# Kernel tuning notes

Hardware: AMD Instinct MI355X
Metric: run time of the kernel (lower is better)

The kernel has to match this reference:

```python
import jax, jax.numpy as jnp
import numpy as np

N, F, U, R, B, M = 8192, 64, 64, 4, 20, 512


def setup_inputs() -> dict:
    key = jax.random.key(0)
    ks = jax.random.split(key, 6)
    features = jax.random.normal(ks[0], (1, N, F), dtype=jnp.float32)
    out_indices = jax.random.randint(ks[1], (1, M), 0, N, dtype=jnp.int64)
    # normalized adjacency per relation; scale keeps activations O(1)
    adjacency = jax.random.uniform(ks[2], (R, N, N), dtype=jnp.float32) / N
    bases = jax.random.normal(ks[3], (F, U, B), dtype=jnp.float32) * (1.0 / np.sqrt(F * B))
    coefficients = jax.random.normal(ks[4], (R, B), dtype=jnp.float32)
    self_kernel = jax.random.normal(ks[5], (F, U), dtype=jnp.float32) * (1.0 / np.sqrt(F))
    bias = jnp.zeros((U,), dtype=jnp.float32)
    return {
        "features": features,
        "out_indices": out_indices,
        "adjacency": adjacency,
        "bases": bases,
        "coefficients": coefficients,
        "self_kernel": self_kernel,
        "bias": bias,
    }


def reference(features, out_indices, adjacency, bases, coefficients, self_kernel, bias):
    # features: (1, N, F); adjacency: (R, N, N)
    x = features[0]  # (N, F) -- full-batch, batch dim is 1
    # basis decomposition: W_r = sum_k bases[:, :, k] * coeff[r, k]
    W = jnp.einsum("fuk,rk->rfu", bases, coefficients)  # (R, F, U)
    xw = jnp.einsum("nf,rfu->rnu", x, W)               # (R, N, U)
    agg = jnp.einsum("rnm,rmu->nu", adjacency, xw)      # sum_r A_r @ (X W_r)
    out = agg + x @ self_kernel + bias                   # (N, U)
    out = jax.nn.relu(out)
    # final_layer=False: return all node features with batch dim restored
    return out[None]  # (1, N, U)
```

## Files before the change

### kernel.cpp

```cpp
#include <hip/hip_runtime.h>


typedef float v4f __attribute__((ext_vector_type(4)));
typedef unsigned int v4u __attribute__((ext_vector_type(4)));
typedef short v8s __attribute__((ext_vector_type(8)));

__device__ __forceinline__ unsigned short f2bf(float f) {
  unsigned int u = __builtin_bit_cast(unsigned int, f);
  return (unsigned short)((u + 0x7fffu + ((u >> 16) & 1u)) >> 16);
}

__device__ __forceinline__ void gload16(const void* g, void* l) {
  __builtin_amdgcn_global_load_lds((const __attribute__((address_space(1))) void*)g,
                                   (__attribute__((address_space(3))) void*)l, 16, 0, 0);
}

__global__ __launch_bounds__(256) void rgcn_wk(const float* __restrict__ bases,
                                               const float* __restrict__ coef,
                                               float* __restrict__ W) {
  int i = blockIdx.x * 256 + threadIdx.x;
  int r = i >> 12;
  int fu = i & 4095;
  float s = 0.f;
#pragma unroll
  for (int k = 0; k < 20; ++k) s += bases[fu * 20 + k] * coef[r * 20 + k];
  W[i] = s;
}

__global__ __launch_bounds__(256) void rgcn_prep(const float* __restrict__ x,
                                                 const float* __restrict__ W,
                                                 const float* __restrict__ sk,
                                                 const float* __restrict__ bias,
                                                 unsigned short* __restrict__ xwf,
                                                 float* __restrict__ selfout) {
  __shared__ float lx[2048];
  __shared__ unsigned short lxw[8192];
  const int t = threadIdx.x;
  const int blk = blockIdx.x;
  const int n0 = blk * 32;
  for (int i = t; i < 2048; i += 256) lx[i] = x[(size_t)n0 * 64 + i];
  __syncthreads();
  const int u = t & 63, rq = t >> 6;
  float acc[8][5];
#pragma unroll
  for (int p = 0; p < 8; ++p)
#pragma unroll
    for (int c = 0; c < 5; ++c) acc[p][c] = 0.f;
  const float* wu = W + u;
  const float* sku = sk + u;
#pragma unroll 4
  for (int f = 0; f < 64; ++f) {
    float w0 = wu[f * 64];
    float w1 = wu[4096 + f * 64];
    float w2 = wu[8192 + f * 64];
    float w3 = wu[12288 + f * 64];
    float w4 = sku[f * 64];
#pragma unroll
    for (int p = 0; p < 8; ++p) {
      float xv = lx[(rq * 8 + p) * 64 + f];
      acc[p][0] += xv * w0;
      acc[p][1] += xv * w1;
      acc[p][2] += xv * w2;
      acc[p][3] += xv * w3;
      acc[p][4] += xv * w4;
    }
  }
  const float bu = bias[u];
#pragma unroll
  for (int p = 0; p < 8; ++p) {
    int km = rq * 8 + p;
    selfout[(size_t)(n0 + km) * 64 + u] = acc[p][4] + bu;
    int idx = (u >> 4) * 512 + ((km >> 3) * 16 + (u & 15)) * 8 + (km & 7);
#pragma unroll
    for (int r = 0; r < 4; ++r) lxw[r * 2048 + idx] = f2bf(acc[p][r]);
  }
  __syncthreads();
  const unsigned int* lsrc = (const unsigned int*)lxw;
  unsigned int* gdst = (unsigned int*)xwf;
  for (int i = t; i < 4096; i += 256) {
    int r = i >> 10, q = i & 1023;
    gdst[(size_t)(r * 256 + blk) * 1024 + q] = lsrc[i];
  }
}


#define PACK8(S, X0, X1)          \
  {                               \
    S[0] = (short)f2bf(X0.x);     \
    S[1] = (short)f2bf(X0.y);     \
    S[2] = (short)f2bf(X0.z);     \
    S[3] = (short)f2bf(X0.w);     \
    S[4] = (short)f2bf(X1.x);     \
    S[5] = (short)f2bf(X1.y);     \
    S[6] = (short)f2bf(X1.z);     \
    S[7] = (short)f2bf(X1.w);     \
  }

#define STAGE(P)                                          \
  {                                                       \
    char* stb = smem + (w * 2 + (P)) * 8192;              \
    gload16(aps0, stb);                                   \
    gload16(aps1, stb + 1024);                            \
    gload16(aps2, stb + 2048);                            \
    gload16(aps3, stb + 3072);                            \
    gload16(bpp, stb + 4096);                             \
    gload16(bpp + 512, stb + 5120);                       \
    gload16(bpp + 1024, stb + 6144);                      \
    gload16(bpp + 1536, stb + 7168);                      \
    aps0 += 32; aps1 += 32; aps2 += 32; aps3 += 32;       \
    bpp += 2048;                                          \
  }

#define STEP(P, VMN, DO_STAGE)                                             \
  {                                                                        \
    asm volatile("s_waitcnt vmcnt(" #VMN ")" ::: "memory");                \
    __builtin_amdgcn_sched_barrier(0);                                     \
    const char* sb = smem + (w * 2 + (P)) * 8192;                          \
    v4f a00 = *(const v4f*)(sb + ao00);                                    \
    v4f a01 = *(const v4f*)(sb + ao01);                                    \
    v4f a10 = *(const v4f*)(sb + ao10);                                    \
    v4f a11 = *(const v4f*)(sb + ao11);                                    \
    v4u b0 = *(const v4u*)(sb + bo);                                       \
    v4u b1 = *(const v4u*)(sb + bo + 1024);                                \
    v4u b2 = *(const v4u*)(sb + bo + 2048);                                \
    v4u b3 = *(const v4u*)(sb + bo + 3072);                                \
    asm volatile("s_waitcnt lgkmcnt(0)" ::: "memory");                     \
    __builtin_amdgcn_sched_barrier(0);                                     \
    if (DO_STAGE) STAGE(P)                                                 \
    v8s af0, af1;                                                          \
    PACK8(af0, a00, a01);                                                  \
    PACK8(af1, a10, a11);                                                  \
    v8s bf0 = __builtin_bit_cast(v8s, b0);                                 \
    v8s bf1 = __builtin_bit_cast(v8s, b1);                                 \
    v8s bf2 = __builtin_bit_cast(v8s, b2);                                 \
    v8s bf3 = __builtin_bit_cast(v8s, b3);                                 \
    acc00 = __builtin_amdgcn_mfma_f32_16x16x32_bf16(af0, bf0, acc00, 0, 0, 0); \
    acc01 = __builtin_amdgcn_mfma_f32_16x16x32_bf16(af0, bf1, acc01, 0, 0, 0); \
    acc02 = __builtin_amdgcn_mfma_f32_16x16x32_bf16(af0, bf2, acc02, 0, 0, 0); \
    acc03 = __builtin_amdgcn_mfma_f32_16x16x32_bf16(af0, bf3, acc03, 0, 0, 0); \
    acc10 = __builtin_amdgcn_mfma_f32_16x16x32_bf16(af1, bf0, acc10, 0, 0, 0); \
    acc11 = __builtin_amdgcn_mfma_f32_16x16x32_bf16(af1, bf1, acc11, 0, 0, 0); \
    acc12 = __builtin_amdgcn_mfma_f32_16x16x32_bf16(af1, bf2, acc12, 0, 0, 0); \
    acc13 = __builtin_amdgcn_mfma_f32_16x16x32_bf16(af1, bf3, acc13, 0, 0, 0); \
  }

#define STORE_FRAG(ACC, RF, UT)                                        \
  red[w][((RF)*16 + lhi * 4 + 0) * 64 + (UT)*16 + l15] = ACC.x;        \
  red[w][((RF)*16 + lhi * 4 + 1) * 64 + (UT)*16 + l15] = ACC.y;        \
  red[w][((RF)*16 + lhi * 4 + 2) * 64 + (UT)*16 + l15] = ACC.z;        \
  red[w][((RF)*16 + lhi * 4 + 3) * 64 + (UT)*16 + l15] = ACC.w;

__global__ __launch_bounds__(256, 1) void rgcn_main(const float* __restrict__ A,
                                                    const unsigned short* __restrict__ xwf,
                                                    float* __restrict__ out) {
  __shared__ __align__(16) char smem[65536];
  const int tid = threadIdx.x;
  const int n0 = blockIdx.x * 32;
  const int w = tid >> 6;
  const int l = tid & 63;
  const int l15 = l & 15, lhi = l >> 4;

  const float* aps0 = A + ((size_t)w * 8192 + (size_t)(n0 + 0 + (l >> 3))) * 8192 + (((l & 7) ^ (l >> 3)) << 2);
  const float* aps1 = aps0 + (size_t)8 * 8192;
  const float* aps2 = aps0 + (size_t)16 * 8192;
  const float* aps3 = aps0 + (size_t)24 * 8192;
  const unsigned short* bpp = xwf + (size_t)(w * 256) * 2048 + (size_t)l * 8;

  const int ao00 = ((0 * 16 + l15) * 8 + ((lhi * 2 + 0) ^ (l15 & 7))) * 16;
  const int ao01 = ((0 * 16 + l15) * 8 + ((lhi * 2 + 1) ^ (l15 & 7))) * 16;
  const int ao10 = ((1 * 16 + l15) * 8 + ((lhi * 2 + 0) ^ (l15 & 7))) * 16;
  const int ao11 = ((1 * 16 + l15) * 8 + ((lhi * 2 + 1) ^ (l15 & 7))) * 16;
  const int bo = 4096 + l * 16;

  v4f acc00 = {0.f, 0.f, 0.f, 0.f}, acc01 = {0.f, 0.f, 0.f, 0.f};
  v4f acc02 = {0.f, 0.f, 0.f, 0.f}, acc03 = {0.f, 0.f, 0.f, 0.f};
  v4f acc10 = {0.f, 0.f, 0.f, 0.f}, acc11 = {0.f, 0.f, 0.f, 0.f};
  v4f acc12 = {0.f, 0.f, 0.f, 0.f}, acc13 = {0.f, 0.f, 0.f, 0.f};

  STAGE(0)
  STAGE(1)
  for (int t = 0; t < 127; ++t) {
    STEP(0, 8, 1)
    STEP(1, 8, 1)
  }
  STEP(0, 8, 0)
  STEP(1, 0, 0)

  __syncthreads();
  float(*red)[2048] = (float(*)[2048])smem;
  STORE_FRAG(acc00, 0, 0)
  STORE_FRAG(acc01, 0, 1)
  STORE_FRAG(acc02, 0, 2)
  STORE_FRAG(acc03, 0, 3)
  STORE_FRAG(acc10, 1, 0)
  STORE_FRAG(acc11, 1, 1)
  STORE_FRAG(acc12, 1, 2)
  STORE_FRAG(acc13, 1, 3)
  __syncthreads();
#pragma unroll
  for (int p = 0; p < 8; ++p) {
    int i = tid + 256 * p;
    float v = red[0][i] + red[1][i] + red[2][i] + red[3][i] + out[(size_t)n0 * 64 + i];
    out[(size_t)n0 * 64 + i] = fmaxf(v, 0.f);
  }
}

extern "C" void kernel_launch(void* const* d_in, const int* in_sizes, int n_in,
                              void* d_out, int out_size, void* d_ws, size_t ws_size,
                              hipStream_t stream) {
  const float* feat = (const float*)d_in[0];
  const float* adj = (const float*)d_in[2];
  const float* bases = (const float*)d_in[3];
  const float* coef = (const float*)d_in[4];
  const float* sk = (const float*)d_in[5];
  const float* bias = (const float*)d_in[6];
  float* out = (float*)d_out;

  unsigned short* xwf = (unsigned short*)d_ws;
  float* W = (float*)((char*)d_ws + (4u << 20));

  rgcn_wk<<<64, 256, 0, stream>>>(bases, coef, W);
  rgcn_prep<<<256, 256, 0, stream>>>(feat, W, sk, bias, xwf, out);
  rgcn_main<<<256, 256, 0, stream>>>(adj, xwf, out);

  (void)in_sizes;
  (void)n_in;
  (void)out_size;
  (void)ws_size;
}
```

Before: 219.5 us.

## Split main GEMM by relation with shared B tile and atomic output reduction

After: 257.2 us. 1.17x slower.

```diff
diff --git a/kernel.cpp b/kernel.cpp
--- a/kernel.cpp
+++ b/kernel.cpp
@@ -98,33 +98,37 @@
 
 #define STAGE(P)                                          \
   {                                                       \
-    char* stb = smem + (w * 2 + (P)) * 8192;              \
-    gload16(aps0, stb);                                   \
-    gload16(aps1, stb + 1024);                            \
-    gload16(aps2, stb + 2048);                            \
-    gload16(aps3, stb + 3072);                            \
-    gload16(bpp, stb + 4096);                             \
-    gload16(bpp + 512, stb + 5120);                       \
-    gload16(bpp + 1024, stb + 6144);                      \
-    gload16(bpp + 1536, stb + 7168);                      \
+    char* ab = Aw + (P)*4096;                             \
+    gload16(aps0, ab);                                    \
+    gload16(aps1, ab + 1024);                             \
+    gload16(aps2, ab + 2048);                             \
+    gload16(aps3, ab + 3072);                             \
+    char* bb = Bb + (P)*4096 + w * 2048;                  \
+    gload16(bsrc, bb);                                    \
+    gload16(bsrc + 512, bb + 1024);                       \
     aps0 += 32; aps1 += 32; aps2 += 32; aps3 += 32;       \
-    bpp += 2048;                                          \
+    bsrc += 2048;                                         \
   }
 
 #define STEP(P, VMN, DO_STAGE)                                             \
   {                                                                        \
     asm volatile("s_waitcnt vmcnt(" #VMN ")" ::: "memory");                \
     __builtin_amdgcn_sched_barrier(0);                                     \
-    const char* sb = smem + (w * 2 + (P)) * 8192;                          \
-    v4f a00 = *(const v4f*)(sb + ao00);                                    \
-    v4f a01 = *(const v4f*)(sb + ao01);                                    \
-    v4f a10 = *(const v4f*)(sb + ao10);                                    \
-    v4f a11 = *(const v4f*)(sb + ao11);                                    \
-    v4u b0 = *(const v4u*)(sb + bo);                                       \
-    v4u b1 = *(const v4u*)(sb + bo + 1024);                                \
-    v4u b2 = *(const v4u*)(sb + bo + 2048);                                \
-    v4u b3 = *(const v4u*)(sb + bo + 3072);                                \
+    __builtin_amdgcn_s_barrier();                                          \
+    __builtin_amdgcn_sched_barrier(0);                                     \
+    const char* ap = Aw + (P)*4096;                                        \
+    const char* bp = Bb + (P)*4096;                                        \
+    v4f a00 = *(const v4f*)(ap + ao00);                                    \
+    v4f a01 = *(const v4f*)(ap + ao01);                                    \
+    v4f a10 = *(const v4f*)(ap + ao10);                                    \
+    v4f a11 = *(const v4f*)(ap + ao11);                                    \
+    v4u b0 = *(const v4u*)(bp + bo);                                       \
+    v4u b1 = *(const v4u*)(bp + bo + 1024);                                \
+    v4u b2 = *(const v4u*)(bp + bo + 2048);                                \
+    v4u b3 = *(const v4u*)(bp + bo + 3072);                                \
     asm volatile("s_waitcnt lgkmcnt(0)" ::: "memory");                     \
+    __builtin_amdgcn_sched_barrier(0);                                     \
+    __builtin_amdgcn_s_barrier();                                          \
     __builtin_amdgcn_sched_barrier(0);                                     \
     if (DO_STAGE) STAGE(P)                                                 \
     v8s af0, af1;                                                          \
@@ -144,65 +148,75 @@
     acc13 = __builtin_amdgcn_mfma_f32_16x16x32_bf16(af1, bf3, acc13, 0, 0, 0); \
   }
 
-#define STORE_FRAG(ACC, RF, UT)                                        \
-  red[w][((RF)*16 + lhi * 4 + 0) * 64 + (UT)*16 + l15] = ACC.x;        \
-  red[w][((RF)*16 + lhi * 4 + 1) * 64 + (UT)*16 + l15] = ACC.y;        \
-  red[w][((RF)*16 + lhi * 4 + 2) * 64 + (UT)*16 + l15] = ACC.z;        \
-  red[w][((RF)*16 + lhi * 4 + 3) * 64 + (UT)*16 + l15] = ACC.w;
+#define ATOM_FRAG(ACC, RF, UT)                                   \
+  atomicAdd(ob + ((RF)*16 + 0) * 64 + (UT)*16, ACC.x);           \
+  atomicAdd(ob + ((RF)*16 + 1) * 64 + (UT)*16, ACC.y);           \
+  atomicAdd(ob + ((RF)*16 + 2) * 64 + (UT)*16, ACC.z);           \
+  atomicAdd(ob + ((RF)*16 + 3) * 64 + (UT)*16, ACC.w);
 
 __global__ __launch_bounds__(256, 1) void rgcn_main(const float* __restrict__ A,
                                                     const unsigned short* __restrict__ xwf,
                                                     float* __restrict__ out) {
-  __shared__ __align__(16) char smem[65536];
+  __shared__ __align__(16) char smem[81920];
   const int tid = threadIdx.x;
-  const int n0 = blockIdx.x * 32;
+  const int r = blockIdx.x & 3;
+  const int n0 = (blockIdx.x >> 2) * 128;
   const int w = tid >> 6;
   const int l = tid & 63;
   const int l15 = l & 15, lhi = l >> 4;
-
-  const float* aps0 = A + ((size_t)w * 8192 + (size_t)(n0 + 0 + (l >> 3))) * 8192 + (((l & 7) ^ (l >> 3)) << 2);
+  const int row0 = n0 + w * 32;
+
+  const float* aps0 = A + ((size_t)r * 8192 + (size_t)(row0 + (l >> 3))) * 8192 + (((l & 7) ^ (l >> 3)) << 2);
   const float* aps1 = aps0 + (size_t)8 * 8192;
   const float* aps2 = aps0 + (size_t)16 * 8192;
   const float* aps3 = aps0 + (size_t)24 * 8192;
-  const unsigned short* bpp = xwf + (size_t)(w * 256) * 2048 + (size_t)l * 8;
+  const unsigned short* bsrc = xwf + (size_t)r * 524288 + (size_t)w * 1024 + (size_t)l * 8;
+
+  char* Aw = smem + w * 16384;
+  char* Bb = smem + 65536;
 
   const int ao00 = ((0 * 16 + l15) * 8 + ((lhi * 2 + 0) ^ (l15 & 7))) * 16;
   const int ao01 = ((0 * 16 + l15) * 8 + ((lhi * 2 + 1) ^ (l15 & 7))) * 16;
   const int ao10 = ((1 * 16 + l15) * 8 + ((lhi * 2 + 0) ^ (l15 & 7))) * 16;
   const int ao11 = ((1 * 16 + l15) * 8 + ((lhi * 2 + 1) ^ (l15 & 7))) * 16;
-  const int bo = 4096 + l * 16;
+  const int bo = l * 16;
 
   v4f acc00 = {0.f, 0.f, 0.f, 0.f}, acc01 = {0.f, 0.f, 0.f, 0.f};
   v4f acc02 = {0.f, 0.f, 0.f, 0.f}, acc03 = {0.f, 0.f, 0.f, 0.f};
   v4f acc10 = {0.f, 0.f, 0.f, 0.f}, acc11 = {0.f, 0.f, 0.f, 0.f};
   v4f acc12 = {0.f, 0.f, 0.f, 0.f}, acc13 = {0.f, 0.f, 0.f, 0.f};
 
-  STAGE(0)
-  STAGE(1)
-  for (int t = 0; t < 127; ++t) {
-    STEP(0, 8, 1)
-    STEP(1, 8, 1)
-  }
-  STEP(0, 8, 0)
-  STEP(1, 0, 0)
-
-  __syncthreads();
-  float(*red)[2048] = (float(*)[2048])smem;
-  STORE_FRAG(acc00, 0, 0)
-  STORE_FRAG(acc01, 0, 1)
-  STORE_FRAG(acc02, 0, 2)
-  STORE_FRAG(acc03, 0, 3)
-  STORE_FRAG(acc10, 1, 0)
-  STORE_FRAG(acc11, 1, 1)
-  STORE_FRAG(acc12, 1, 2)
-  STORE_FRAG(acc13, 1, 3)
-  __syncthreads();
-#pragma unroll
-  for (int p = 0; p < 8; ++p) {
-    int i = tid + 256 * p;
-    float v = red[0][i] + red[1][i] + red[2][i] + red[3][i] + out[(size_t)n0 * 64 + i];
-    out[(size_t)n0 * 64 + i] = fmaxf(v, 0.f);
-  }
+  STAGE(0) STAGE(1) STAGE(2) STAGE(3)
+  for (int t = 0; t < 63; ++t) {
+    STEP(0, 18, 1)
+    STEP(1, 18, 1)
+    STEP(2, 18, 1)
+    STEP(3, 18, 1)
+  }
+  STEP(0, 18, 0)
+  STEP(1, 12, 0)
+  STEP(2, 6, 0)
+  STEP(3, 0, 0)
+
+  float* ob = out + ((size_t)row0 + lhi * 4) * 64 + l15;
+  ATOM_FRAG(acc00, 0, 0)
+  ATOM_FRAG(acc01, 0, 1)
+  ATOM_FRAG(acc02, 0, 2)
+  ATOM_FRAG(acc03, 0, 3)
+  ATOM_FRAG(acc10, 1, 0)
+  ATOM_FRAG(acc11, 1, 1)
+  ATOM_FRAG(acc12, 1, 2)
+  ATOM_FRAG(acc13, 1, 3)
+}
+
+__global__ __launch_bounds__(256) void rgcn_relu(float* __restrict__ out) {
+  int i = blockIdx.x * 256 + threadIdx.x;
+  v4f v = ((v4f*)out)[i];
+  v.x = fmaxf(v.x, 0.f);
+  v.y = fmaxf(v.y, 0.f);
+  v.z = fmaxf(v.z, 0.f);
+  v.w = fmaxf(v.w, 0.f);
+  ((v4f*)out)[i] = v;
 }
 
 extern "C" void kernel_launch(void* const* d_in, const int* in_sizes, int n_in,
@@ -222,6 +236,7 @@
   rgcn_wk<<<64, 256, 0, stream>>>(bases, coef, W);
   rgcn_prep<<<256, 256, 0, stream>>>(feat, W, sk, bias, xwf, out);
   rgcn_main<<<256, 256, 0, stream>>>(adj, xwf, out);
+  rgcn_relu<<<512, 256, 0, stream>>>(out);
 
   (void)in_sizes;
   (void)n_in;
```
